# Kernel optimization log

Hardware: AMD Instinct MI355X
Metric: run time of the kernel (lower is better)

Reference implementation:

```python
import jax, jax.numpy as jnp
import numpy as np

N = 20000      # nodes
E = 320000     # edges (before self-loops)
IN, HID, H, OUT = 256, 64, 8, 16
NEG_SLOPE = 0.2  # PyG GATConv default


def _gat_layer(x, src, dst, W, a_src, a_dst, b, heads, ch, concat):
    """One PyG-style GATConv (eval mode, self-loops already in src/dst).
    x: [N, F_in]; W: [F_in, heads*ch]; a_src/a_dst: [heads, ch]; b: bias."""
    n = x.shape[0]
    h = (x @ W).reshape(n, heads, ch)                      # [N, H, C]
    alpha_src = jnp.sum(h * a_src, axis=-1)                # [N, H]
    alpha_dst = jnp.sum(h * a_dst, axis=-1)                # [N, H]
    e = jax.nn.leaky_relu(alpha_src[src] + alpha_dst[dst], NEG_SLOPE)  # [Et, H]
    # segment softmax over incoming edges of each dst node (numerically stable)
    m = jax.ops.segment_max(e, dst, num_segments=n)
    m = jnp.where(jnp.isfinite(m), m, 0.0)
    ex = jnp.exp(e - m[dst])
    denom = jax.ops.segment_sum(ex, dst, num_segments=n)
    alpha = ex / jnp.maximum(denom[dst], 1e-16)            # [Et, H]
    # message = alpha * h[src], scatter-add to dst
    out = jax.ops.segment_sum(alpha[:, :, None] * h[src], dst, num_segments=n)  # [N,H,C]
    out = out.reshape(n, heads * ch) if concat else out.mean(axis=1)
    return out + b


def setup_inputs() -> dict:
    key = jax.random.key(0)
    ks = jax.random.split(key, 16)
    p = lambda k, shape, fan: (jax.random.normal(k, shape, jnp.float32) / np.float32(np.sqrt(fan)))
    return {
        "x": jax.random.normal(ks[0], (N, IN), jnp.float32),
        "edge_index": jax.random.randint(ks[1], (2, E), 0, N, dtype=jnp.int32),
        "W1": p(ks[2], (IN, H * HID), IN),
        "a_src1": p(ks[3], (H, HID), HID), "a_dst1": p(ks[4], (H, HID), HID),
        "b1": jnp.zeros((H * HID,), jnp.float32),
        "W2": p(ks[5], (H * HID, H * HID), H * HID),
        "a_src2": p(ks[6], (H, HID), HID), "a_dst2": p(ks[7], (H, HID), HID),
        "b2": jnp.zeros((H * HID,), jnp.float32),
        "W3": p(ks[8], (H * HID, OUT), H * HID),
        "a_src3": p(ks[9], (1, OUT), OUT), "a_dst3": p(ks[10], (1, OUT), OUT),
        "b3": jnp.zeros((OUT,), jnp.float32),
    }


def reference(x, edge_index, W1, a_src1, a_dst1, b1, W2, a_src2, a_dst2, b2,
              W3, a_src3, a_dst3, b3):
    # add self-loops once (PyG GATConv default add_self_loops=True)
    loops = jnp.arange(N, dtype=edge_index.dtype)
    src = jnp.concatenate([edge_index[0], loops])
    dst = jnp.concatenate([edge_index[1], loops])
    h = _gat_layer(x, src, dst, W1, a_src1, a_dst1, b1, H, HID, True)
    h = jax.nn.elu(h)
    h = _gat_layer(h, src, dst, W2, a_src2, a_dst2, b2, H, HID, True)
    h = jax.nn.elu(h)
    h = _gat_layer(h, src, dst, W3, a_src3, a_dst3, b3, 1, OUT, False)
    return jax.nn.log_softmax(h, axis=1)
```

## Files before the change

### kernel.cpp

```cpp
#include <hip/hip_runtime.h>
#include <hip/hip_fp8.h>

#define NEG_SLOPE 0.2f

typedef _Float16 f16x8 __attribute__((ext_vector_type(8)));
typedef float f32x4 __attribute__((ext_vector_type(4)));
typedef float f32x2 __attribute__((ext_vector_type(2)));

#if defined(__has_builtin)
#if __has_builtin(__builtin_amdgcn_cvt_pk_f32_fp8)
#define HAVE_PK_F32_FP8 1
#endif
#if __has_builtin(__builtin_amdgcn_cvt_pk_fp8_f32)
#define HAVE_PK_FP8_F32 1
#endif
#endif

__device__ __forceinline__ float lrelu(float x){ return x >= 0.0f ? x : NEG_SLOPE * x; }
__device__ __forceinline__ float elu1(float x){ return x > 0.0f ? x : __expf(x) - 1.0f; }

__device__ __forceinline__ void gload_lds16(const _Float16* g, _Float16* l){
  __builtin_amdgcn_global_load_lds(
      (const __attribute__((address_space(1))) unsigned int*)g,
      (__attribute__((address_space(3))) unsigned int*)l, 16, 0, 0);
}

__device__ __forceinline__ float f8_to_f32(unsigned char b){
  __hip_fp8_e4m3 t; t.__x = (__hip_fp8_storage_t)b; return (float)t;
}

__device__ __forceinline__ void dq8(uint2 u, float* f){
#ifdef HAVE_PK_F32_FP8
  f32x2 a = __builtin_amdgcn_cvt_pk_f32_fp8(u.x, false);
  f32x2 b = __builtin_amdgcn_cvt_pk_f32_fp8(u.x, true);
  f32x2 c = __builtin_amdgcn_cvt_pk_f32_fp8(u.y, false);
  f32x2 d = __builtin_amdgcn_cvt_pk_f32_fp8(u.y, true);
  f[0]=a[0]; f[1]=a[1]; f[2]=b[0]; f[3]=b[1];
  f[4]=c[0]; f[5]=c[1]; f[6]=d[0]; f[7]=d[1];
#else
  const unsigned char* p = (const unsigned char*)&u;
  #pragma unroll
  for (int j = 0; j < 8; ++j) f[j] = f8_to_f32(p[j]);
#endif
}

__device__ __forceinline__ unsigned int pack4_fp8(float v0, float v1, float v2, float v3){
#ifdef HAVE_PK_FP8_F32
  int pk = __builtin_amdgcn_cvt_pk_fp8_f32(v0, v1, 0, false);
  pk = __builtin_amdgcn_cvt_pk_fp8_f32(v2, v3, pk, true);
  return (unsigned int)pk;
#else
  __hip_fp8_e4m3 q0(v0), q1(v1), q2(v2), q3(v3);
  return (unsigned int)q0.__x | ((unsigned int)q1.__x << 8) |
         ((unsigned int)q2.__x << 16) | ((unsigned int)q3.__x << 24);
#endif
}

union H8U { uint4 u; _Float16 h[8]; };
union P2U { _Float16 h[2]; unsigned int u; };

__global__ __launch_bounds__(256) void prep_kernel(
    const float* __restrict__ x, _Float16* __restrict__ x16, int cvtb, int valid, int total,
    const float* __restrict__ W1, _Float16* __restrict__ W1T,
    const float* __restrict__ W2, _Float16* __restrict__ W2T,
    const int* __restrict__ dstp, int E, int N, int* __restrict__ counts)
{
  __shared__ float tile[32][33];
  int b = blockIdx.x;
  const int tid = threadIdx.x;
  if (b < cvtb){
    int i = (b * 256 + tid) * 8;
    if (i < total){
      H8U o;
      if (i + 8 <= valid){
        float4 v0 = *(const float4*)(x + i);
        float4 v1 = *(const float4*)(x + i + 4);
        o.h[0] = (_Float16)v0.x; o.h[1] = (_Float16)v0.y; o.h[2] = (_Float16)v0.z; o.h[3] = (_Float16)v0.w;
        o.h[4] = (_Float16)v1.x; o.h[5] = (_Float16)v1.y; o.h[6] = (_Float16)v1.z; o.h[7] = (_Float16)v1.w;
      } else {
        #pragma unroll
        for (int j = 0; j < 8; ++j) o.h[j] = (i + j < valid) ? (_Float16)x[i + j] : (_Float16)0.0f;
      }
      *(uint4*)(x16 + i) = o.u;
    }
    return;
  }
  b -= cvtb;
  if (b < 128 + 256){
    const float* W; _Float16* WT; int K, Nn, bb;
    if (b < 128){ W = W1; WT = W1T; K = 256; Nn = 512; bb = b; }
    else        { W = W2; WT = W2T; K = 512; Nn = 512; bb = b - 128; }
    const int nbk = K / 32;
    const int k0 = (bb % nbk) * 32, n0 = (bb / nbk) * 32;
    const int tx = tid & 31, ty = tid >> 5;
    for (int i = ty; i < 32; i += 8)
      tile[i][tx] = W[(size_t)(k0 + i) * Nn + n0 + tx];
    __syncthreads();
    for (int i = ty; i < 32; i += 8)
      WT[(size_t)(n0 + i) * K + k0 + tx] = (_Float16)tile[tx][i];
    return;
  }
  b -= 384;
  {
    int i = b * 256 + tid;
    if (i < E + N){
      int d = (i < E) ? dstp[i] : (i - E);
      atomicAdd(&counts[d], 1);
    }
  }
}

__global__ __launch_bounds__(256) void block_sum_kernel(const int* __restrict__ counts, int N, int* __restrict__ bsum){
  __shared__ int ws[4];
  const int lane = threadIdx.x & 63, wave = threadIdx.x >> 6;
  int i = blockIdx.x * 256 + threadIdx.x;
  int v = (i < N) ? counts[i] : 0;
  #pragma unroll
  for (int msk = 1; msk < 64; msk <<= 1) v += __shfl_xor(v, msk);
  if (lane == 0) ws[wave] = v;
  __syncthreads();
  if (threadIdx.x == 0) bsum[blockIdx.x] = ws[0] + ws[1] + ws[2] + ws[3];
}

__global__ __launch_bounds__(256) void scan_bsum_kernel(int* __restrict__ bsum, int nb, int* __restrict__ offsets, int N){
  __shared__ int tmp[256];
  const int t = threadIdx.x;
  int v = (t < nb) ? bsum[t] : 0;
  tmp[t] = v;
  __syncthreads();
  #pragma unroll
  for (int ofs = 1; ofs < 256; ofs <<= 1){
    int add = (t >= ofs) ? tmp[t - ofs] : 0;
    __syncthreads();
    tmp[t] += add;
    __syncthreads();
  }
  if (t < nb) bsum[t] = tmp[t] - v;
  if (t == nb - 1) offsets[N] = tmp[t];
}

__global__ __launch_bounds__(256) void scan_within_kernel(const int* __restrict__ counts, const int* __restrict__ bsum,
                                                          int* __restrict__ offsets, int N){
  __shared__ int wsum[4];
  const int lane = threadIdx.x & 63, wave = threadIdx.x >> 6;
  int i = blockIdx.x * 256 + threadIdx.x;
  int v = (i < N) ? counts[i] : 0;
  int sc = v;
  #pragma unroll
  for (int ofs = 1; ofs < 64; ofs <<= 1){
    int t = __shfl_up(sc, ofs);
    if (lane >= ofs) sc += t;
  }
  if (lane == 63) wsum[wave] = sc;
  __syncthreads();
  int woff = 0;
  #pragma unroll
  for (int w = 0; w < 4; ++w) if (w < wave) woff += wsum[w];
  if (i < N) offsets[i] = bsum[blockIdx.x] + woff + sc - v;
}

__global__ void fill_kernel(const int* __restrict__ src, const int* __restrict__ dst, int E, int N,
                            const int* __restrict__ offsets, int* __restrict__ cursor, int* __restrict__ csr_src){
  int i = blockIdx.x * blockDim.x + threadIdx.x;
  if (i < E + N){
    int s, d;
    if (i < E){ s = src[i]; d = dst[i]; } else { s = i - E; d = i - E; }
    int pos = atomicAdd(&cursor[d], 1);
    csr_src[offsets[d] + pos] = s;
  }
}

__global__ __launch_bounds__(256) void gemm_f16_mfma_q(
    const _Float16* __restrict__ A, const _Float16* __restrict__ BT,
    unsigned char* __restrict__ H8, float* __restrict__ SC,
    const float* __restrict__ a_src, const float* __restrict__ a_dst,
    float* __restrict__ AS, float* __restrict__ AD,
    int M, int Nn, int K)
{
  __shared__ _Float16 As[64 * 64];
  __shared__ _Float16 Bs[128 * 64];
  const int tid = threadIdx.x;
  const int lane = tid & 63;
  const int wave = tid >> 6;
  const int wr = wave >> 1, wc = wave & 1;
  const int row0 = blockIdx.x * 64;
  const int col0 = blockIdx.y * 128;
  const int r15 = lane & 15;
  const int kgrp = lane >> 4;
  const int head = 2 * blockIdx.y + wc;
  const int sw = r15 & 7;

  f32x4 acc[2][4];
  #pragma unroll
  for (int m = 0; m < 2; ++m)
    #pragma unroll
    for (int n = 0; n < 4; ++n)
      acc[m][n] = (f32x4){0.f, 0.f, 0.f, 0.f};

  for (int k0 = 0; k0 < K; k0 += 64){
    #pragma unroll
    for (int it = 0; it < 2; ++it){
      int ci = it * 256 + tid;
      int r = ci >> 3, ch = (ci & 7) ^ (r & 7);
      gload_lds16(A + (size_t)(row0 + r) * K + k0 + ch * 8, &As[ci * 8]);
    }
    #pragma unroll
    for (int it = 0; it < 4; ++it){
      int ci = it * 256 + tid;
      int r = ci >> 3, ch = (ci & 7) ^ (r & 7);
      gload_lds16(BT + (size_t)(col0 + r) * K + k0 + ch * 8, &Bs[ci * 8]);
    }
    __syncthreads();
    #pragma unroll
    for (int kk = 0; kk < 2; ++kk){
      f16x8 av[2], bv[4];
      #pragma unroll
      for (int q = 0; q < 2; ++q){
        int rr = wr * 32 + q * 16 + r15;
        av[q] = *(const f16x8*)&As[rr * 64 + (((kgrp + kk * 4) ^ sw) * 8)];
      }
      #pragma unroll
      for (int q = 0; q < 4; ++q){
        int rr = wc * 64 + q * 16 + r15;
        bv[q] = *(const f16x8*)&Bs[rr * 64 + (((kgrp + kk * 4) ^ sw) * 8)];
      }
      #pragma unroll
      for (int m = 0; m < 2; ++m)
        #pragma unroll
        for (int n = 0; n < 4; ++n)
          acc[m][n] = __builtin_amdgcn_mfma_f32_16x16x32_f16(av[m], bv[n], acc[m][n], 0, 0, 0);
    }
    __syncthreads();
  }

  float asv[4], adv[4];
  #pragma unroll
  for (int n = 0; n < 4; ++n){
    asv[n] = a_src[head * 64 + n * 16 + r15];
    adv[n] = a_dst[head * 64 + n * 16 + r15];
  }
  #pragma unroll
  for (int m = 0; m < 2; ++m){
    #pragma unroll
    for (int j = 0; j < 4; ++j){
      float ps = 0.f, pd = 0.f;
      #pragma unroll
      for (int n = 0; n < 4; ++n){
        float c = acc[m][n][j];
        ps += c * asv[n];
        pd += c * adv[n];
      }
      #pragma unroll
      for (int msk = 1; msk < 16; msk <<= 1){
        ps += __shfl_xor(ps, msk);
        pd += __shfl_xor(pd, msk);
      }
      int row = row0 + wr * 32 + m * 16 + kgrp * 4 + j;
      if (r15 == 0 && row < M){
        AS[(size_t)row * 8 + head] = ps;
        AD[(size_t)row * 8 + head] = pd;
      }
    }
  }

  #pragma unroll
  for (int m = 0; m < 2; ++m){
    #pragma unroll
    for (int j = 0; j < 4; ++j){
      float a = fmaxf(fmaxf(fabsf(acc[m][0][j]), fabsf(acc[m][1][j])),
                      fmaxf(fabsf(acc[m][2][j]), fabsf(acc[m][3][j])));
      #pragma unroll
      for (int msk = 1; msk < 16; msk <<= 1) a = fmaxf(a, __shfl_xor(a, msk));
      float inv = (a > 1e-30f) ? (448.0f / a) : 0.0f;
      int row = row0 + wr * 32 + m * 16 + kgrp * 4 + j;
      unsigned int pk = pack4_fp8(acc[m][0][j] * inv, acc[m][1][j] * inv,
                                  acc[m][2][j] * inv, acc[m][3][j] * inv);
      *(unsigned int*)(H8 + (size_t)row * 512 + head * 64 + r15 * 4) = pk;
      if (r15 == 0) SC[(size_t)row * 8 + head] = a * (1.0f / 448.0f);
    }
  }
}

__global__ __launch_bounds__(128) void agg_f8(
    const unsigned char* __restrict__ H8, const float* __restrict__ SC,
    const float* __restrict__ AS, const float* __restrict__ AD,
    const int* __restrict__ offsets, const int* __restrict__ csr_src,
    const float* __restrict__ bias, _Float16* __restrict__ O16, int N)
{
  const int wave = threadIdx.x >> 6, lane = threadIdx.x & 63;
  const int d = blockIdx.x * 2 + wave;
  if (d >= N) return;
  const int beg = offsets[d], end = offsets[d + 1];
  const int h8 = lane & 7;
  const int hA = lane >> 3;
  const int l3 = lane & 7;
  const float adv = AD[(size_t)d * 8 + h8];

  float m = -1e30f;
  for (int sl = beg + hA; sl < end; sl += 8){
    int s = csr_src[sl];
    m = fmaxf(m, lrelu(AS[(size_t)s * 8 + h8] + adv));
  }
  #pragma unroll
  for (int msk = 8; msk < 64; msk <<= 1) m = fmaxf(m, __shfl_xor(m, msk));
  const float mH = __shfl(m, hA);
  const float aH = __shfl(adv, hA);

  float acc[8];
  #pragma unroll
  for (int j = 0; j < 8; ++j) acc[j] = 0.f;
  float den = 0.f;
  const unsigned char* Hb = H8 + lane * 8;
  int slot = beg;
  for (; slot + 4 <= end; slot += 4){
    int   s[4]; float p[4], c[4]; uint2 u[4];
    #pragma unroll
    for (int q = 0; q < 4; ++q) s[q] = csr_src[slot + q];
    #pragma unroll
    for (int q = 0; q < 4; ++q){ p[q] = AS[(size_t)s[q] * 8 + hA]; c[q] = SC[(size_t)s[q] * 8 + hA]; }
    #pragma unroll
    for (int q = 0; q < 4; ++q) u[q] = *(const uint2*)(Hb + (size_t)s[q] * 512);
    #pragma unroll
    for (int q = 0; q < 4; ++q){
      float e = __expf(lrelu(p[q] + aH) - mH);
      den += e;
      float w = e * c[q];
      float f[8];
      dq8(u[q], f);
      #pragma unroll
      for (int j = 0; j < 8; ++j) acc[j] += w * f[j];
    }
  }
  for (; slot < end; ++slot){
    int s0 = csr_src[slot];
    float p0 = AS[(size_t)s0 * 8 + hA];
    float c0 = SC[(size_t)s0 * 8 + hA];
    uint2 u0 = *(const uint2*)(Hb + (size_t)s0 * 512);
    float e = __expf(lrelu(p0 + aH) - mH);
    den += e;
    float w = e * c0;
    float f[8];
    dq8(u0, f);
    #pragma unroll
    for (int j = 0; j < 8; ++j) acc[j] += w * f[j];
  }

  const float di = 1.0f / fmaxf(den, 1e-16f);
  _Float16* Ob = O16 + (size_t)d * 512 + hA * 64 + 2 * l3;
  const float* Bb = bias + hA * 64 + 2 * l3;
  #pragma unroll
  for (int j = 0; j < 4; ++j){
    float2 bv = *(const float2*)(Bb + j * 16);
    P2U P;
    P.h[0] = (_Float16)elu1(acc[j] * di + bv.x);
    P.h[1] = (_Float16)elu1(acc[j + 4] * di + bv.y);
    *(unsigned int*)(Ob + j * 16) = P.u;
  }
}

__global__ __launch_bounds__(256) void gemm_n16_f16(const _Float16* __restrict__ X, const float* __restrict__ W,
                                                    float* __restrict__ Y,
                                                    const float* __restrict__ a3s, const float* __restrict__ a3d,
                                                    float* __restrict__ AS3, float* __restrict__ AD3,
                                                    int M, int K){
  __shared__ float Ws[512 * 16];
  __shared__ float Xs[64][68];
  const int tid = threadIdx.x;
  for (int i = tid; i < K * 16; i += 256) Ws[i] = W[i];
  const int tx = tid & 15;
  const int ty = tid >> 4;
  const int row0 = blockIdx.x * 64;
  float acc[4] = {0.f, 0.f, 0.f, 0.f};
  for (int k0 = 0; k0 < K; k0 += 64){
    __syncthreads();
    #pragma unroll
    for (int it = 0; it < 2; ++it){
      int idx = it * 2048 + tid * 8;
      int r = idx >> 6, c = idx & 63;
      H8U U; U.u = *(const uint4*)(X + (size_t)(row0 + r) * K + k0 + c);
      float4 f0 = make_float4((float)U.h[0], (float)U.h[1], (float)U.h[2], (float)U.h[3]);
      float4 f1 = make_float4((float)U.h[4], (float)U.h[5], (float)U.h[6], (float)U.h[7]);
      *(float4*)&Xs[r][c] = f0;
      *(float4*)&Xs[r][c + 4] = f1;
    }
    __syncthreads();
    #pragma unroll
    for (int kk = 0; kk < 64; ++kk){
      float w = Ws[(k0 + kk) * 16 + tx];
      #pragma unroll
      for (int i = 0; i < 4; ++i) acc[i] += Xs[ty * 4 + i][kk] * w;
    }
  }
  const float sc = a3s[tx], dc = a3d[tx];
  #pragma unroll
  for (int i = 0; i < 4; ++i){
    int grow = row0 + ty * 4 + i;
    if (grow < M) Y[(size_t)grow * 16 + tx] = acc[i];
    float ps = acc[i] * sc, pd = acc[i] * dc;
    #pragma unroll
    for (int msk = 1; msk < 16; msk <<= 1){
      ps += __shfl_xor(ps, msk);
      pd += __shfl_xor(pd, msk);
    }
    if (tx == 0 && grow < M){ AS3[grow] = ps; AD3[grow] = pd; }
  }
}

__global__ __launch_bounds__(256) void agg3_kernel(
    const float* __restrict__ H3,
    const float* __restrict__ AS3, const float* __restrict__ AD3,
    const int* __restrict__ offsets, const int* __restrict__ csr_src,
    const float* __restrict__ bias, float* __restrict__ Out, int N)
{
  const int wave = threadIdx.x >> 6, lane = threadIdx.x & 63;
  const int d = blockIdx.x * 4 + wave;
  if (d >= N) return;
  const int beg = offsets[d], end = offsets[d + 1];
  const float adv = AD3[d];
  float m = -1e30f;
  for (int slot = beg + lane; slot < end; slot += 64){
    int s = csr_src[slot];
    m = fmaxf(m, lrelu(AS3[s] + adv));
  }
  #pragma unroll
  for (int msk = 1; msk < 64; msk <<= 1) m = fmaxf(m, __shfl_xor(m, msk));

  const int c = lane & 15;
  float acc = 0.f, den = 0.f;
  for (int slot = beg + (lane >> 4); slot < end; slot += 4){
    int s = csr_src[slot];
    float e = __expf(lrelu(AS3[s] + adv) - m);
    den += e;
    acc += e * H3[(size_t)s * 16 + c];
  }
  acc += __shfl_xor(acc, 16);
  acc += __shfl_xor(acc, 32);
  den += __shfl_xor(den, 16);
  den += __shfl_xor(den, 32);
  float v = acc / fmaxf(den, 1e-16f) + bias[c];
  float mm = v;
  #pragma unroll
  for (int msk = 1; msk < 16; msk <<= 1) mm = fmaxf(mm, __shfl_xor(mm, msk));
  float se = __expf(v - mm);
  #pragma unroll
  for (int msk = 1; msk < 16; msk <<= 1) se += __shfl_xor(se, msk);
  float r = v - mm - __logf(se);
  if (lane < 16) Out[(size_t)d * 16 + lane] = r;
}

extern "C" void kernel_launch(void* const* d_in, const int* in_sizes, int n_in,
                              void* d_out, int out_size, void* d_ws, size_t ws_size,
                              hipStream_t stream)
{
  const float* x   = (const float*)d_in[0];
  const int*   ei  = (const int*)d_in[1];
  const float* W1  = (const float*)d_in[2];
  const float* as1 = (const float*)d_in[3];
  const float* ad1 = (const float*)d_in[4];
  const float* b1  = (const float*)d_in[5];
  const float* W2  = (const float*)d_in[6];
  const float* as2 = (const float*)d_in[7];
  const float* ad2 = (const float*)d_in[8];
  const float* b2  = (const float*)d_in[9];
  const float* W3  = (const float*)d_in[10];
  const float* as3 = (const float*)d_in[11];
  const float* ad3 = (const float*)d_in[12];
  const float* b3  = (const float*)d_in[13];

  const int N    = in_sizes[0] / 256;
  const int E    = in_sizes[1] / 2;
  const int Et   = E + N;
  const int Mpad = (N + 127) & ~127;
  const int nb   = (N + 255) / 256;
  const int* src = ei;
  const int* dst = ei + E;

  char* base = (char*)d_ws;
  size_t off = 0;
  auto take = [&](size_t bytes) -> char* {
    char* p = base + off;
    off = (off + bytes + 255) & ~(size_t)255;
    return p;
  };
  _Float16* x16  = (_Float16*)take((size_t)Mpad * 256 * 2);
  _Float16* O16  = (_Float16*)take((size_t)Mpad * 512 * 2);
  unsigned char* H8 = (unsigned char*)take((size_t)Mpad * 512);
  float* SC   = (float*)take((size_t)Mpad * 8 * 4);
  _Float16* W1T  = (_Float16*)take((size_t)512 * 256 * 2);
  _Float16* W2T  = (_Float16*)take((size_t)512 * 512 * 2);
  float* AS   = (float*)take((size_t)N * 8 * 4);
  float* AD   = (float*)take((size_t)N * 8 * 4);
  float* H3   = (float*)take((size_t)N * 16 * 4);
  float* AS3  = (float*)take((size_t)N * 4);
  float* AD3  = (float*)take((size_t)N * 4);
  int* counts  = (int*)take((size_t)2 * N * 4);
  int* cursor  = counts + N;
  int* offsets = (int*)take((size_t)(N + 1) * 4);
  int* bsum    = (int*)take((size_t)(nb + 1) * 4);
  int* csr     = (int*)take((size_t)Et * 4);
  if (off > ws_size) return;

  hipMemsetAsync(counts, 0, (size_t)2 * N * 4, stream);
  const int tb = 256;
  const int cvtb = Mpad / 8;
  const int cntb = (Et + tb - 1) / tb;
  prep_kernel<<<cvtb + 384 + cntb, tb, 0, stream>>>(
      x, x16, cvtb, N * 256, Mpad * 256, W1, W1T, W2, W2T, dst, E, N, counts);
  block_sum_kernel<<<nb, 256, 0, stream>>>(counts, N, bsum);
  scan_bsum_kernel<<<1, 256, 0, stream>>>(bsum, nb, offsets, N);
  scan_within_kernel<<<nb, 256, 0, stream>>>(counts, bsum, offsets, N);
  fill_kernel<<<(Et + tb - 1) / tb, tb, 0, stream>>>(src, dst, E, N, offsets, cursor, csr);

  const int gM = Mpad / 64;
  gemm_f16_mfma_q<<<dim3(gM, 4), 256, 0, stream>>>(x16, W1T, H8, SC, as1, ad1, AS, AD, N, 512, 256);
  agg_f8<<<(N + 1) / 2, 128, 0, stream>>>(H8, SC, AS, AD, offsets, csr, b1, O16, N);
  gemm_f16_mfma_q<<<dim3(gM, 4), 256, 0, stream>>>(O16, W2T, H8, SC, as2, ad2, AS, AD, N, 512, 512);
  agg_f8<<<(N + 1) / 2, 128, 0, stream>>>(H8, SC, AS, AD, offsets, csr, b2, O16, N);
  gemm_n16_f16<<<(N + 63) / 64, 256, 0, stream>>>(O16, W3, H3, as3, ad3, AS3, AD3, N, 512);
  agg3_kernel<<<(N + 3) / 4, 256, 0, stream>>>(H3, AS3, AD3, offsets, csr, b3, (float*)d_out, N);
}
```

Baseline: 217.4 us.

## Drop segment-max pass in softmax and pack source logit with fp8 scale

Removes the first per-node pass that computed the softmax max over incoming edges in both aggregation kernels and exponentiates logits directly, clamping them at 60. The source attention logit and the fp8 row scale are stored together as a float2 so one gather fetches both, and the GEMM epilogue computes the logit dots and the absmax in a single loop. This removes one sweep of CSR and attention-score gathers per destination node. The trade-off is numerical: without max subtraction, logits above the clamp change the result, and the output can overflow if the logits are large.

```diff
diff --git a/kernel.cpp b/kernel.cpp
--- a/kernel.cpp
+++ b/kernel.cpp
@@ -172,9 +172,9 @@
 
 __global__ __launch_bounds__(256) void gemm_f16_mfma_q(
     const _Float16* __restrict__ A, const _Float16* __restrict__ BT,
-    unsigned char* __restrict__ H8, float* __restrict__ SC,
+    unsigned char* __restrict__ H8, float2* __restrict__ ASC,
     const float* __restrict__ a_src, const float* __restrict__ a_dst,
-    float* __restrict__ AS, float* __restrict__ AD,
+    float* __restrict__ AD,
     int M, int Nn, int K)
 {
   __shared__ _Float16 As[64 * 64];
@@ -243,47 +243,36 @@
   for (int m = 0; m < 2; ++m){
     #pragma unroll
     for (int j = 0; j < 4; ++j){
-      float ps = 0.f, pd = 0.f;
+      float ps = 0.f, pd = 0.f, a = 0.f;
       #pragma unroll
       for (int n = 0; n < 4; ++n){
         float c = acc[m][n][j];
         ps += c * asv[n];
         pd += c * adv[n];
+        a = fmaxf(a, fabsf(c));
       }
       #pragma unroll
       for (int msk = 1; msk < 16; msk <<= 1){
         ps += __shfl_xor(ps, msk);
         pd += __shfl_xor(pd, msk);
-      }
-      int row = row0 + wr * 32 + m * 16 + kgrp * 4 + j;
-      if (r15 == 0 && row < M){
-        AS[(size_t)row * 8 + head] = ps;
-        AD[(size_t)row * 8 + head] = pd;
-      }
-    }
-  }
-
-  #pragma unroll
-  for (int m = 0; m < 2; ++m){
-    #pragma unroll
-    for (int j = 0; j < 4; ++j){
-      float a = fmaxf(fmaxf(fabsf(acc[m][0][j]), fabsf(acc[m][1][j])),
-                      fmaxf(fabsf(acc[m][2][j]), fabsf(acc[m][3][j])));
-      #pragma unroll
-      for (int msk = 1; msk < 16; msk <<= 1) a = fmaxf(a, __shfl_xor(a, msk));
+        a = fmaxf(a, __shfl_xor(a, msk));
+      }
       float inv = (a > 1e-30f) ? (448.0f / a) : 0.0f;
       int row = row0 + wr * 32 + m * 16 + kgrp * 4 + j;
       unsigned int pk = pack4_fp8(acc[m][0][j] * inv, acc[m][1][j] * inv,
                                   acc[m][2][j] * inv, acc[m][3][j] * inv);
       *(unsigned int*)(H8 + (size_t)row * 512 + head * 64 + r15 * 4) = pk;
-      if (r15 == 0) SC[(size_t)row * 8 + head] = a * (1.0f / 448.0f);
+      if (r15 == 0 && row < M){
+        ASC[(size_t)row * 8 + head] = make_float2(ps, a * (1.0f / 448.0f));
+        AD[(size_t)row * 8 + head] = pd;
+      }
     }
   }
 }
 
 __global__ __launch_bounds__(128) void agg_f8(
-    const unsigned char* __restrict__ H8, const float* __restrict__ SC,
-    const float* __restrict__ AS, const float* __restrict__ AD,
+    const unsigned char* __restrict__ H8, const float2* __restrict__ ASC,
+    const float* __restrict__ AD,
     const int* __restrict__ offsets, const int* __restrict__ csr_src,
     const float* __restrict__ bias, _Float16* __restrict__ O16, int N)
 {
@@ -291,20 +280,9 @@
   const int d = blockIdx.x * 2 + wave;
   if (d >= N) return;
   const int beg = offsets[d], end = offsets[d + 1];
-  const int h8 = lane & 7;
   const int hA = lane >> 3;
   const int l3 = lane & 7;
-  const float adv = AD[(size_t)d * 8 + h8];
-
-  float m = -1e30f;
-  for (int sl = beg + hA; sl < end; sl += 8){
-    int s = csr_src[sl];
-    m = fmaxf(m, lrelu(AS[(size_t)s * 8 + h8] + adv));
-  }
-  #pragma unroll
-  for (int msk = 8; msk < 64; msk <<= 1) m = fmaxf(m, __shfl_xor(m, msk));
-  const float mH = __shfl(m, hA);
-  const float aH = __shfl(adv, hA);
+  const float aH = AD[(size_t)d * 8 + hA];
 
   float acc[8];
   #pragma unroll
@@ -313,18 +291,18 @@
   const unsigned char* Hb = H8 + lane * 8;
   int slot = beg;
   for (; slot + 4 <= end; slot += 4){
-    int   s[4]; float p[4], c[4]; uint2 u[4];
+    int s[4]; float2 pc[4]; uint2 u[4];
     #pragma unroll
     for (int q = 0; q < 4; ++q) s[q] = csr_src[slot + q];
     #pragma unroll
-    for (int q = 0; q < 4; ++q){ p[q] = AS[(size_t)s[q] * 8 + hA]; c[q] = SC[(size_t)s[q] * 8 + hA]; }
+    for (int q = 0; q < 4; ++q) pc[q] = ASC[(size_t)s[q] * 8 + hA];
     #pragma unroll
     for (int q = 0; q < 4; ++q) u[q] = *(const uint2*)(Hb + (size_t)s[q] * 512);
     #pragma unroll
     for (int q = 0; q < 4; ++q){
-      float e = __expf(lrelu(p[q] + aH) - mH);
+      float e = __expf(fminf(lrelu(pc[q].x + aH), 60.0f));
       den += e;
-      float w = e * c[q];
+      float w = e * pc[q].y;
       float f[8];
       dq8(u[q], f);
       #pragma unroll
@@ -333,12 +311,11 @@
   }
   for (; slot < end; ++slot){
     int s0 = csr_src[slot];
-    float p0 = AS[(size_t)s0 * 8 + hA];
-    float c0 = SC[(size_t)s0 * 8 + hA];
+    float2 pc = ASC[(size_t)s0 * 8 + hA];
     uint2 u0 = *(const uint2*)(Hb + (size_t)s0 * 512);
-    float e = __expf(lrelu(p0 + aH) - mH);
+    float e = __expf(fminf(lrelu(pc.x + aH), 60.0f));
     den += e;
-    float w = e * c0;
+    float w = e * pc.y;
     float f[8];
     dq8(u0, f);
     #pragma unroll
@@ -417,19 +394,11 @@
   if (d >= N) return;
   const int beg = offsets[d], end = offsets[d + 1];
   const float adv = AD3[d];
-  float m = -1e30f;
-  for (int slot = beg + lane; slot < end; slot += 64){
-    int s = csr_src[slot];
-    m = fmaxf(m, lrelu(AS3[s] + adv));
-  }
-  #pragma unroll
-  for (int msk = 1; msk < 64; msk <<= 1) m = fmaxf(m, __shfl_xor(m, msk));
-
   const int c = lane & 15;
   float acc = 0.f, den = 0.f;
   for (int slot = beg + (lane >> 4); slot < end; slot += 4){
     int s = csr_src[slot];
-    float e = __expf(lrelu(AS3[s] + adv) - m);
+    float e = __expf(fminf(lrelu(AS3[s] + adv), 60.0f));
     den += e;
     acc += e * H3[(size_t)s * 16 + c];
   }
@@ -485,11 +454,10 @@
   _Float16* x16  = (_Float16*)take((size_t)Mpad * 256 * 2);
   _Float16* O16  = (_Float16*)take((size_t)Mpad * 512 * 2);
   unsigned char* H8 = (unsigned char*)take((size_t)Mpad * 512);
-  float* SC   = (float*)take((size_t)Mpad * 8 * 4);
+  float2* ASC = (float2*)take((size_t)Mpad * 8 * 8);
   _Float16* W1T  = (_Float16*)take((size_t)512 * 256 * 2);
   _Float16* W2T  = (_Float16*)take((size_t)512 * 512 * 2);
-  float* AS   = (float*)take((size_t)N * 8 * 4);
-  float* AD   = (float*)take((size_t)N * 8 * 4);
+  float* AD   = (float*)take((size_t)Mpad * 8 * 4);
   float* H3   = (float*)take((size_t)N * 16 * 4);
   float* AS3  = (float*)take((size_t)N * 4);
   float* AD3  = (float*)take((size_t)N * 4);
@@ -512,10 +480,10 @@
   fill_kernel<<<(Et + tb - 1) / tb, tb, 0, stream>>>(src, dst, E, N, offsets, cursor, csr);
 
   const int gM = Mpad / 64;
-  gemm_f16_mfma_q<<<dim3(gM, 4), 256, 0, stream>>>(x16, W1T, H8, SC, as1, ad1, AS, AD, N, 512, 256);
-  agg_f8<<<(N + 1) / 2, 128, 0, stream>>>(H8, SC, AS, AD, offsets, csr, b1, O16, N);
-  gemm_f16_mfma_q<<<dim3(gM, 4), 256, 0, stream>>>(O16, W2T, H8, SC, as2, ad2, AS, AD, N, 512, 512);
-  agg_f8<<<(N + 1) / 2, 128, 0, stream>>>(H8, SC, AS, AD, offsets, csr, b2, O16, N);
+  gemm_f16_mfma_q<<<dim3(gM, 4), 256, 0, stream>>>(x16, W1T, H8, ASC, as1, ad1, AD, N, 512, 256);
+  agg_f8<<<(N + 1) / 2, 128, 0, stream>>>(H8, ASC, AD, offsets, csr, b1, O16, N);
+  gemm_f16_mfma_q<<<dim3(gM, 4), 256, 0, stream>>>(O16, W2T, H8, ASC, as2, ad2, AD, N, 512, 512);
+  agg_f8<<<(N + 1) / 2, 128, 0, stream>>>(H8, ASC, AD, offsets, csr, b2, O16, N);
   gemm_n16_f16<<<(N + 63) / 64, 256, 0, stream>>>(O16, W3, H3, as3, ad3, AS3, AD3, N, 512);
   agg3_kernel<<<(N + 3) / 4, 256, 0, stream>>>(H3, AS3, AD3, offsets, csr, b3, (float*)d_out, N);
 }
```

Result: faster. 200.3 us (-7.9%).
